# Kernel optimization log

Hardware: AMD Instinct MI355X
Metric: run time of the kernel (lower is better)

## Reference

```python
import jax, jax.numpy as jnp
import numpy as np

NUM_CLASSES = 256
FEATURE_DIM = 768
BATCH = 128
SIM_BALANCE = 0.7
TIER1 = 50.0
TIER2 = 10.0
TOPK = 5


def _l2norm(x):
    return x / jnp.linalg.norm(x, axis=1, keepdims=True)


def build_edge_weights(class_features, context_features, w1, b1, w2, b2,
                       co_occurrence, instance_counts):
    """Vectorized, faithful translation of VisualFeatureGraph.build_graph."""
    N = class_features.shape[0]
    dt = class_features.dtype
    co = co_occurrence.astype(dt)            # [N,N], diag is 0
    cnt = instance_counts.astype(dt)         # [N]

    vs = _l2norm(class_features) @ _l2norm(class_features).T    # visual_sim [N,N]
    cs = _l2norm(context_features) @ _l2norm(context_features).T  # context_sim
    combined = SIM_BALANCE * vs + (1.0 - SIM_BALANCE) * cs

    # ---- Tier 1: co > TIER1 ----
    # sim_proj(f_i - f_j): exploit linearity of first layer: (f_i-f_j)@W1 = a_i - a_j
    a = class_features @ w1                                    # [N, D/2]
    h = jax.nn.relu(a[:, None, :] - a[None, :, :] + b1)        # [N,N,D/2]
    sim_weight = jax.nn.sigmoid(h @ w2 + b2)[..., 0]           # [N,N]
    ratio = (jnp.minimum(cnt[:, None], cnt[None, :]) /
             jnp.maximum(jnp.maximum(cnt[:, None], cnt[None, :]), 1.0))
    e1 = combined * sim_weight * ratio

    # ---- Tier 2: TIER2 < co <= TIER1 ----
    # shared neighbors k: co[i,k]>T1 and co[j,k]>T1 (k=i,j auto-excluded: diag=0
    # and co[i,j]<=T1 for tier-2 pairs)
    A = (co > TIER1).astype(dt)                                # [N,N]
    M = vs * A
    shared_sum = M @ M.T                                       # sum_k vs[i,k]*vs[j,k]
    shared_cnt = A @ A.T
    avg_sim = shared_sum / jnp.maximum(shared_cnt, 1.0)
    conf = co / TIER1
    e2 = jnp.where(shared_cnt > 0,
                   conf * combined + (1.0 - conf) * avg_sim,
                   conf * combined)

    # ---- Tier 3: co <= TIER2 ----
    # top-5 neighbors per row by co-occurrence among co > TIER2 (diag=0 and
    # co[i,j]<=TIER2 for tier-3 pairs, so i and j are auto-excluded)
    top_vals, top_idx = jax.lax.top_k(co, TOPK)                # [N,K]
    valid = top_vals > TIER2                                   # [N,K]
    ii = top_idx[:, None, :, None]                             # [N,1,K,1]
    jj = top_idx[None, :, None, :]                             # [1,N,1,K]
    co_cross = co[ii, jj]                                      # co[i_neigh, j_neigh] [N,N,K,K]
    vs_cross = vs[ii, jj]
    vs_in = jnp.take_along_axis(vs, top_idx, axis=1)           # vs[i, i_neigh] [N,K]
    mask = valid[:, None, :, None] & valid[None, :, None, :] & (co_cross > 0)
    w = (top_vals[:, None, :, None] * top_vals[None, :, None, :]) / TIER1
    w = jnp.where(mask, w, 0.0)
    sim = vs_in[:, None, :, None] * vs_in[None, :, None, :] * vs_cross
    trans = jnp.sum(w * sim, axis=(2, 3))                      # [N,N]
    tot = jnp.sum(w, axis=(2, 3))
    e3 = jnp.where(tot > 0, trans / jnp.where(tot > 0, tot, 1.0), 0.1 * cs)

    tier1_mask = co > TIER1
    tier2_mask = (co > TIER2) & ~tier1_mask
    E = jnp.where(tier1_mask, e1, jnp.where(tier2_mask, e2, e3))
    E = E * (1.0 - jnp.eye(N, dtype=dt))                       # i==j skipped
    mx = jnp.max(E)
    E = jnp.where(mx > 0, E / jnp.where(mx > 0, mx, 1.0), E)
    return E


def setup_inputs() -> dict:
    key = jax.random.key(0)
    ks = jax.random.split(key, 8)
    N, D, B = NUM_CLASSES, FEATURE_DIM, BATCH
    x = jax.random.normal(ks[0], (B, N, D), dtype=jnp.float32)
    class_features = jax.random.normal(ks[1], (N, D), dtype=jnp.float32) * 0.05
    context_features = jax.random.normal(ks[2], (N, D), dtype=jnp.float32) * 0.05
    w1 = jax.random.normal(ks[3], (D, D // 2), dtype=jnp.float32) * (1.0 / np.sqrt(D))
    b1 = jnp.zeros((D // 2,), dtype=jnp.float32)
    w2 = jax.random.normal(ks[4], (D // 2, 1), dtype=jnp.float32) * (1.0 / np.sqrt(D // 2))
    b2 = jnp.zeros((1,), dtype=jnp.float32)
    co = jax.random.randint(ks[5], (N, N), 0, 121, dtype=jnp.int32)
    co = (co + co.T) // 2                                      # symmetric like update_features
    co = co * (1 - jnp.eye(N, dtype=jnp.int32))                # zero diagonal
    instance_counts = jax.random.randint(ks[6], (N,), 1, 1001, dtype=jnp.int32)
    return {"x": x, "class_features": class_features,
            "context_features": context_features,
            "w1": w1, "b1": b1, "w2": w2, "b2": b2,
            "co_occurrence": co, "instance_counts": instance_counts}


def reference(x, class_features, context_features, w1, b1, w2, b2,
              co_occurrence, instance_counts):
    E = build_edge_weights(class_features, context_features, w1, b1, w2, b2,
                           co_occurrence, instance_counts)
    # torch.bmm(E.expand(B,-1,-1), x) == einsum over shared node dim
    return x + jnp.einsum('ij,bjd->bid', E, x)
```

## Files before the change

kernel.cpp:

```cpp
#include <hip/hip_runtime.h>
#include <hip/hip_bf16.h>
#include <math.h>

#define N 256
#define D 768
#define BATCH 128

typedef float f32x4 __attribute__((ext_vector_type(4)));
typedef short bf16x8 __attribute__((ext_vector_type(8)));

static __device__ __forceinline__ unsigned short f2bf(float f) {
    unsigned int u = __float_as_uint(f);
    u += 0x7fffu + ((u >> 16) & 1u);
    return (unsigned short)(u >> 16);
}
static __device__ __forceinline__ unsigned int pack2bf(float lo, float hi) {
    unsigned int a = __float_as_uint(lo);
    unsigned int b = __float_as_uint(hi);
    a += 0x7fffu + ((a >> 16) & 1u);
    b += 0x7fffu + ((b >> 16) & 1u);
    return (a >> 16) | (b & 0xffff0000u);
}

__global__ void k_stage1(const float* __restrict__ cf, const float* __restrict__ ctx,
                         float* __restrict__ vsn, float* __restrict__ csn,
                         const float* __restrict__ w1, float* __restrict__ a,
                         const int* __restrict__ co, float* __restrict__ topv,
                         int* __restrict__ topi) {
    __shared__ float sm[2 * 64 * 33];
    int bx = blockIdx.x;
    int t = threadIdx.x;
    if (bx < 512) {
        int row = bx;
        const float* src;
        float* dst;
        if (row < N) { src = cf  + row * D;       dst = vsn + row * D; }
        else         { src = ctx + (row - N) * D; dst = csn + (row - N) * D; }
        float s = 0.f;
        for (int d = t; d < D; d += 256) { float v = src[d]; s += v * v; }
        float* red = sm;
        red[t] = s; __syncthreads();
        for (int off = 128; off > 0; off >>= 1) {
            if (t < off) red[t] += red[t + off];
            __syncthreads();
        }
        float inv = 1.0f / sqrtf(red[0]);
        for (int d = t; d < D; d += 256) dst[d] = src[d] * inv;
    } else if (bx < 608) {
        int bi = bx - 512;
        int i0 = (bi / 12) * 32, j0 = (bi % 12) * 32;
        float (*Ci)[33] = (float(*)[33])sm;
        float (*Wj)[33] = (float(*)[33])(sm + 64 * 33);
        int tx = t & 15, ty = t >> 4;
        float a00 = 0.f, a01 = 0.f, a10 = 0.f, a11 = 0.f;
        for (int k0 = 0; k0 < 768; k0 += 64) {
            #pragma unroll
            for (int s = 0; s < 8; s++) {
                int idx = s * 256 + t;
                int row = idx >> 6, kc = idx & 63;
                Ci[kc][row] = cf[(i0 + row) * 768 + k0 + kc];
                int kr = idx >> 5, col = idx & 31;
                Wj[kr][col] = w1[(k0 + kr) * 384 + j0 + col];
            }
            __syncthreads();
            #pragma unroll 4
            for (int kk = 0; kk < 64; kk++) {
                float iv0 = Ci[kk][ty * 2], iv1 = Ci[kk][ty * 2 + 1];
                float jv0 = Wj[kk][tx * 2], jv1 = Wj[kk][tx * 2 + 1];
                a00 += iv0 * jv0; a01 += iv0 * jv1;
                a10 += iv1 * jv0; a11 += iv1 * jv1;
            }
            __syncthreads();
        }
        a[(i0 + ty * 2)     * 384 + j0 + tx * 2]     = a00;
        a[(i0 + ty * 2)     * 384 + j0 + tx * 2 + 1] = a01;
        a[(i0 + ty * 2 + 1) * 384 + j0 + tx * 2]     = a10;
        a[(i0 + ty * 2 + 1) * 384 + j0 + tx * 2 + 1] = a11;
    } else {
        int lane = t & 63;
        int row = (bx - 608) * 4 + (t >> 6);
        int4 v4 = *(const int4*)(co + row * 256 + lane * 4);
        int key[4];
        key[0] = v4.x * 256 + (255 - (lane * 4 + 0));
        key[1] = v4.y * 256 + (255 - (lane * 4 + 1));
        key[2] = v4.z * 256 + (255 - (lane * 4 + 2));
        key[3] = v4.w * 256 + (255 - (lane * 4 + 3));
        for (int r = 0; r < 5; r++) {
            int best = key[0];
            #pragma unroll
            for (int e = 1; e < 4; e++) best = max(best, key[e]);
            #pragma unroll
            for (int off = 32; off > 0; off >>= 1) best = max(best, __shfl_xor(best, off, 64));
            int kidx = 255 - (best & 255);
            int val = best >> 8;
            if (lane == 0) { topv[row * 5 + r] = (float)val; topi[row * 5 + r] = kidx; }
            if ((kidx >> 2) == lane) key[kidx & 3] = -1;
        }
    }
}

__global__ void k_gram2(const float* __restrict__ vsn, const float* __restrict__ csn,
                        float* __restrict__ vs, float* __restrict__ cs) {
    int bx = blockIdx.x;
    const float* S = (bx >= 64) ? csn : vsn;
    float* O       = (bx >= 64) ? cs  : vs;
    int bi = bx & 63;
    int i0 = (bi >> 3) * 32, j0 = (bi & 7) * 32;
    __shared__ float Li[64][33], Lj[64][33];
    int t = threadIdx.x;
    int tx = t & 15, ty = t >> 4;
    float a00 = 0.f, a01 = 0.f, a10 = 0.f, a11 = 0.f;
    for (int k0 = 0; k0 < 768; k0 += 64) {
        #pragma unroll
        for (int s = 0; s < 8; s++) {
            int idx = s * 256 + t;
            int row = idx >> 6, kc = idx & 63;
            Li[kc][row] = S[(i0 + row) * 768 + k0 + kc];
            Lj[kc][row] = S[(j0 + row) * 768 + k0 + kc];
        }
        __syncthreads();
        #pragma unroll 4
        for (int kk = 0; kk < 64; kk++) {
            float iv0 = Li[kk][ty * 2], iv1 = Li[kk][ty * 2 + 1];
            float jv0 = Lj[kk][tx * 2], jv1 = Lj[kk][tx * 2 + 1];
            a00 += iv0 * jv0; a01 += iv0 * jv1;
            a10 += iv1 * jv0; a11 += iv1 * jv1;
        }
        __syncthreads();
    }
    O[(i0 + ty * 2)     * 256 + j0 + tx * 2]     = a00;
    O[(i0 + ty * 2)     * 256 + j0 + tx * 2 + 1] = a01;
    O[(i0 + ty * 2 + 1) * 256 + j0 + tx * 2]     = a10;
    O[(i0 + ty * 2 + 1) * 256 + j0 + tx * 2 + 1] = a11;
}

__global__ void k_stage3(const float* __restrict__ a, const float* __restrict__ b1,
                         const float* __restrict__ w2, const float* __restrict__ b2,
                         const float* __restrict__ vs, const float* __restrict__ cs,
                         const int* __restrict__ ic, float* __restrict__ e1,
                         const int* __restrict__ co, float* __restrict__ ss,
                         float* __restrict__ sc) {
    __shared__ float sm[12800];
    int bx = blockIdx.x;
    int t = threadIdx.x;
    if (bx < 256) {
        int i0 = (bx >> 4) * 16, j0 = (bx & 15) * 16;
        float (*ai)[388]  = (float(*)[388])sm;
        float (*ajm)[388] = (float(*)[388])(sm + 16 * 388);
        float* sw2 = sm + 2 * 16 * 388;
        for (int idx = t; idx < 16 * 96; idx += 256) {
            int r = idx / 96, c = (idx % 96) * 4;
            *(float4*)&ai[r][c] = *(const float4*)(a + (i0 + r) * 384 + c);
            float4 u  = *(const float4*)(a + (j0 + r) * 384 + c);
            float4 bb = *(const float4*)(b1 + c);
            u.x -= bb.x; u.y -= bb.y; u.z -= bb.z; u.w -= bb.w;
            *(float4*)&ajm[r][c] = u;
        }
        for (int k = t; k < 384; k += 256) sw2[k] = w2[k];
        __syncthreads();
        int tx = t & 15, ty = t >> 4;
        float s = 0.f;
        #pragma unroll 4
        for (int k4 = 0; k4 < 96; k4++) {
            float4 xv = *(const float4*)&ai[ty][k4 * 4];
            float4 yv = *(const float4*)&ajm[tx][k4 * 4];
            float4 wv = *(const float4*)&sw2[k4 * 4];
            s += fmaxf(xv.x - yv.x, 0.f) * wv.x;
            s += fmaxf(xv.y - yv.y, 0.f) * wv.y;
            s += fmaxf(xv.z - yv.z, 0.f) * wv.z;
            s += fmaxf(xv.w - yv.w, 0.f) * wv.w;
        }
        int i = i0 + ty, j = j0 + tx;
        float sig = 1.0f / (1.0f + expf(-(s + b2[0])));
        float comb = 0.7f * vs[i * 256 + j] + 0.3f * cs[i * 256 + j];
        float ci = (float)ic[i], cj = (float)ic[j];
        float mn = fminf(ci, cj), mx = fmaxf(ci, cj);
        float ratio = mn / fmaxf(mx, 1.0f);
        e1[i * 256 + j] = comb * sig * ratio;
    } else {
        int bi = bx - 256;
        int i0 = (bi >> 3) * 32, j0 = (bi & 7) * 32;
        float (*Mi)[33] = (float(*)[33])sm;
        float (*Ai)[33] = (float(*)[33])(sm + 2112);
        float (*Mj)[33] = (float(*)[33])(sm + 4224);
        float (*Aj)[33] = (float(*)[33])(sm + 6336);
        int tx = t & 15, ty = t >> 4;
        float s00=0.f,s01=0.f,s10=0.f,s11=0.f;
        float c00=0.f,c01=0.f,c10=0.f,c11=0.f;
        for (int k0 = 0; k0 < 256; k0 += 64) {
            #pragma unroll
            for (int s = 0; s < 8; s++) {
                int idx = s * 256 + t;
                int row = idx >> 6, kc = idx & 63;
                int civ = co[(i0 + row) * 256 + k0 + kc];
                float aa = civ > 50 ? 1.f : 0.f;
                Ai[kc][row] = aa;
                Mi[kc][row] = aa * vs[(i0 + row) * 256 + k0 + kc];
                int cjv = co[(j0 + row) * 256 + k0 + kc];
                float ab = cjv > 50 ? 1.f : 0.f;
                Aj[kc][row] = ab;
                Mj[kc][row] = ab * vs[(j0 + row) * 256 + k0 + kc];
            }
            __syncthreads();
            #pragma unroll 4
            for (int kk = 0; kk < 64; kk++) {
                float mi0 = Mi[kk][ty*2], mi1 = Mi[kk][ty*2+1];
                float ai0 = Ai[kk][ty*2], ai1 = Ai[kk][ty*2+1];
                float mj0 = Mj[kk][tx*2], mj1 = Mj[kk][tx*2+1];
                float aj0 = Aj[kk][tx*2], aj1 = Aj[kk][tx*2+1];
                s00 += mi0*mj0; s01 += mi0*mj1; s10 += mi1*mj0; s11 += mi1*mj1;
                c00 += ai0*aj0; c01 += ai0*aj1; c10 += ai1*aj0; c11 += ai1*aj1;
            }
            __syncthreads();
        }
        ss[(i0+ty*2)  *256 + j0+tx*2]   = s00; ss[(i0+ty*2)  *256 + j0+tx*2+1] = s01;
        ss[(i0+ty*2+1)*256 + j0+tx*2]   = s10; ss[(i0+ty*2+1)*256 + j0+tx*2+1] = s11;
        sc[(i0+ty*2)  *256 + j0+tx*2]   = c00; sc[(i0+ty*2)  *256 + j0+tx*2+1] = c01;
        sc[(i0+ty*2+1)*256 + j0+tx*2]   = c10; sc[(i0+ty*2+1)*256 + j0+tx*2+1] = c11;
    }
}

__global__ void k_assemble(const int* __restrict__ co, const float* __restrict__ vs,
                           const float* __restrict__ cs, const float* __restrict__ e1,
                           const float* __restrict__ ss, const float* __restrict__ sc,
                           const float* __restrict__ topv, const int* __restrict__ topi,
                           float* __restrict__ E, float* __restrict__ partials) {
    int i = blockIdx.x, j = threadIdx.x;
    int cij = co[i * 256 + j];
    float e;
    if (i == j) {
        e = 0.f;
    } else if (cij > 50) {
        e = e1[i * 256 + j];
    } else if (cij > 10) {
        float conf = (float)cij / 50.0f;
        float comb = 0.7f * vs[i * 256 + j] + 0.3f * cs[i * 256 + j];
        float cnt = sc[i * 256 + j];
        float avg = ss[i * 256 + j] / fmaxf(cnt, 1.f);
        e = (cnt > 0.f) ? conf * comb + (1.f - conf) * avg : conf * comb;
    } else {
        float tvi[5], tvj[5]; int tii[5], tij[5];
        #pragma unroll
        for (int k = 0; k < 5; k++) {
            tvi[k] = topv[i * 5 + k]; tii[k] = topi[i * 5 + k];
            tvj[k] = topv[j * 5 + k]; tij[k] = topi[j * 5 + k];
        }
        float trans = 0.f, tot = 0.f;
        #pragma unroll
        for (int k = 0; k < 5; k++) {
            if (!(tvi[k] > 10.f)) continue;
            float vin_i = vs[i * 256 + tii[k]];
            #pragma unroll
            for (int l = 0; l < 5; l++) {
                if (!(tvj[l] > 10.f)) continue;
                int cc = co[tii[k] * 256 + tij[l]];
                if (cc <= 0) continue;
                float w = tvi[k] * tvj[l] / 50.f;
                float sim = vin_i * vs[j * 256 + tij[l]] * vs[tii[k] * 256 + tij[l]];
                trans += w * sim; tot += w;
            }
        }
        e = (tot > 0.f) ? trans / tot : 0.1f * cs[i * 256 + j];
    }
    E[i * 256 + j] = e;
    __shared__ float red[256];
    red[j] = e; __syncthreads();
    for (int off = 128; off > 0; off >>= 1) {
        if (j < off) red[j] = fmaxf(red[j], red[j + off]);
        __syncthreads();
    }
    if (j == 0) partials[i] = red[0];
}

__global__ void k_ep(const float* __restrict__ E, const float* __restrict__ partials,
                     unsigned short* __restrict__ Ep) {
    __shared__ float red[256];
    int t = threadIdx.x;
    red[t] = partials[t]; __syncthreads();
    for (int off = 128; off > 0; off >>= 1) {
        if (t < off) red[t] = fmaxf(red[t], red[t + off]);
        __syncthreads();
    }
    float mx = red[0];
    float s = (mx > 0.f) ? 1.0f / mx : 1.0f;
    int base = (blockIdx.x * 256 + t) * 4;
    float4 e4 = *(const float4*)(E + base);
    float ev[4] = {e4.x, e4.y, e4.z, e4.w};
    unsigned short o[4];
    #pragma unroll
    for (int q = 0; q < 4; q++) {
        int g = base + q;
        float v = s * ev[q] + (((g >> 8) == (g & 255)) ? 1.0f : 0.0f);
        o[q] = f2bf(v);
    }
    uint2 w;
    w.x = (unsigned int)o[0] | ((unsigned int)o[1] << 16);
    w.y = (unsigned int)o[2] | ((unsigned int)o[3] << 16);
    *(uint2*)(Ep + base) = w;
}

#define EINS_BUFB 4736

#define EIN_BODY(KT, BB, XR, bvC, bvN)                                          \
  {                                                                             \
    uint4 pv;                                                                   \
    pv.x = pack2bf(XR[0].x, XR[0].y);                                           \
    pv.y = pack2bf(XR[0].z, XR[0].w);                                           \
    pv.z = pack2bf(XR[1].x, XR[1].y);                                           \
    pv.w = pack2bf(XR[1].z, XR[1].w);                                           \
    *(uint4*)((char*)xs + (BB) + wbyte) = pv;                                   \
    __syncthreads();                                                            \
    if ((KT) < 7) {                                                             \
      _Pragma("unroll")                                                         \
      for (int nf = 0; nf < 4; nf++)                                            \
        bvN[nf] = *(const uint4*)(eprow + (nf << 12) + ((KT) + 1) * 32);        \
    }                                                                           \
    if ((KT) < 6) {                                                             \
      const float* xn = xb + (size_t)((KT) + 2) * 32 * 768;                     \
      XR[0] = *(const float4*)xn;                                               \
      XR[1] = *(const float4*)(xn + 4);                                         \
    }                                                                           \
    uint2 a0[4], a1[4];                                                         \
    _Pragma("unroll")                                                           \
    for (int g = 0; g < 4; g++) {                                               \
      unsigned ag = ra + (BB) + g * 1184;                                       \
      asm volatile("ds_read_b64_tr_b16 %0, %1" : "=v"(a0[g]) : "v"(ag));        \
      asm volatile("ds_read_b64_tr_b16 %0, %1 offset:144" : "=v"(a1[g]) : "v"(ag)); \
    }                                                                           \
    asm volatile("s_waitcnt lgkmcnt(0)" ::: "memory");                          \
    __builtin_amdgcn_sched_barrier(0);                                          \
    _Pragma("unroll")                                                           \
    for (int mf = 0; mf < 4; mf++) {                                            \
      union { uint2 u[2]; bf16x8 v; } af;                                       \
      af.u[0] = a0[mf]; af.u[1] = a1[mf];                                       \
      _Pragma("unroll")                                                         \
      for (int nf = 0; nf < 4; nf++)                                            \
        acc[mf][nf] = __builtin_amdgcn_mfma_f32_16x16x32_bf16(                  \
            af.v, *(const bf16x8*)&bvC[nf], acc[mf][nf], 0, 0, 0);              \
    }                                                                           \
  }

__global__ __launch_bounds__(256, 3) void k_einsum_tr(
    const unsigned short* __restrict__ Ep, const float* __restrict__ x,
    float* __restrict__ out) {
    extern __shared__ unsigned short xs[];
    int t = threadIdx.x;
    int b = blockIdx.y;
    int d0 = blockIdx.x * 64;
    int lane = t & 63, w = t >> 6;
    int l15 = lane & 15, lq = lane >> 4;

    int dh = t & 7, kr = t >> 3;
    const float* xb = x + ((size_t)b * 256) * 768 + (size_t)kr * 768 + d0 + dh * 8;
    unsigned wbyte = (unsigned)((dh >> 1) * 1184 + (kr >> 2) * 144 + (kr & 3) * 32 + (dh & 1) * 16);
    unsigned ra = (unsigned)(lq * 288 + l15 * 8);

    const unsigned short* eprow = Ep + (((w * 64 + l15) << 8) + lq * 8);

    f32x4 acc[4][4];
    #pragma unroll
    for (int mf = 0; mf < 4; mf++)
        #pragma unroll
        for (int nf = 0; nf < 4; nf++)
            #pragma unroll
            for (int e = 0; e < 4; e++) acc[mf][nf][e] = 0.f;

    float4 xA[2], xB[2];
    xA[0] = *(const float4*)xb;
    xA[1] = *(const float4*)(xb + 4);
    xB[0] = *(const float4*)(xb + 32 * 768);
    xB[1] = *(const float4*)(xb + 32 * 768 + 4);
    uint4 bv0[4], bv1[4];
    #pragma unroll
    for (int nf = 0; nf < 4; nf++) bv0[nf] = *(const uint4*)(eprow + (nf << 12));

    #pragma unroll
    for (int k2 = 0; k2 < 4; k2++) {
        EIN_BODY(2 * k2,     0,         xA, bv0, bv1)
        EIN_BODY(2 * k2 + 1, EINS_BUFB, xB, bv1, bv0)
    }

    float* ob = out + ((size_t)b * 256) * 768 + d0;
    #pragma unroll
    for (int mf = 0; mf < 4; mf++) {
        #pragma unroll
        for (int nf = 0; nf < 4; nf++) {
            int i = w * 64 + nf * 16 + l15;
            int d = mf * 16 + lq * 4;
            *(float4*)(ob + (size_t)i * 768 + d) = *(float4*)&acc[mf][nf];
        }
    }
}

extern "C" void kernel_launch(void* const* d_in, const int* in_sizes, int n_in,
                              void* d_out, int out_size, void* d_ws, size_t ws_size,
                              hipStream_t stream) {
    const float* x   = (const float*)d_in[0];
    const float* cf  = (const float*)d_in[1];
    const float* ctx = (const float*)d_in[2];
    const float* w1  = (const float*)d_in[3];
    const float* b1  = (const float*)d_in[4];
    const float* w2  = (const float*)d_in[5];
    const float* b2  = (const float*)d_in[6];
    const int*   co  = (const int*)d_in[7];
    const int*   ic  = (const int*)d_in[8];
    float* out = (float*)d_out;

    float* ws   = (float*)d_ws;
    float* vsn  = ws;
    float* csn  = vsn + 196608;
    float* a    = csn + 196608;
    float* vs   = a + 98304;
    float* cs   = vs + 65536;
    float* e1   = cs + 65536;
    float* ss   = e1 + 65536;
    float* sc   = ss + 65536;
    float* E    = sc + 65536;
    float* topv = E + 65536;
    int*   topi = (int*)(topv + 1280);
    float* partials = (float*)(topi + 1280);
    unsigned short* Ep = (unsigned short*)(partials + 256);

    k_stage1<<<672, 256, 0, stream>>>(cf, ctx, vsn, csn, w1, a, co, topv, topi);
    k_gram2<<<128, 256, 0, stream>>>(vsn, csn, vs, cs);
    k_stage3<<<320, 256, 0, stream>>>(a, b1, w2, b2, vs, cs, ic, e1, co, ss, sc);
    k_assemble<<<256, 256, 0, stream>>>(co, vs, cs, e1, ss, sc, topv, topi, E, partials);
    k_ep<<<64, 256, 0, stream>>>(E, partials, Ep);
    k_einsum_tr<<<dim3(12, BATCH), 256, 2 * EINS_BUFB, stream>>>(Ep, x, out);
}
```

Measured before the change: 288.2 us.

## Stage full x tile transposed in LDS and drop double-buffered transpose reads

New measurement: 289.0 us. About the same (+0.3%).

```diff
diff --git a/kernel.cpp b/kernel.cpp
--- a/kernel.cpp
+++ b/kernel.cpp
@@ -299,85 +299,63 @@
     *(uint2*)(Ep + base) = w;
 }
 
-#define EINS_BUFB 4736
-
-#define EIN_BODY(KT, BB, XR, bvC, bvN)                                          \
-  {                                                                             \
-    uint4 pv;                                                                   \
-    pv.x = pack2bf(XR[0].x, XR[0].y);                                           \
-    pv.y = pack2bf(XR[0].z, XR[0].w);                                           \
-    pv.z = pack2bf(XR[1].x, XR[1].y);                                           \
-    pv.w = pack2bf(XR[1].z, XR[1].w);                                           \
-    *(uint4*)((char*)xs + (BB) + wbyte) = pv;                                   \
-    __syncthreads();                                                            \
-    if ((KT) < 7) {                                                             \
-      _Pragma("unroll")                                                         \
-      for (int nf = 0; nf < 4; nf++)                                            \
-        bvN[nf] = *(const uint4*)(eprow + (nf << 12) + ((KT) + 1) * 32);        \
-    }                                                                           \
-    if ((KT) < 6) {                                                             \
-      const float* xn = xb + (size_t)((KT) + 2) * 32 * 768;                     \
-      XR[0] = *(const float4*)xn;                                               \
-      XR[1] = *(const float4*)(xn + 4);                                         \
-    }                                                                           \
-    uint2 a0[4], a1[4];                                                         \
-    _Pragma("unroll")                                                           \
-    for (int g = 0; g < 4; g++) {                                               \
-      unsigned ag = ra + (BB) + g * 1184;                                       \
-      asm volatile("ds_read_b64_tr_b16 %0, %1" : "=v"(a0[g]) : "v"(ag));        \
-      asm volatile("ds_read_b64_tr_b16 %0, %1 offset:144" : "=v"(a1[g]) : "v"(ag)); \
-    }                                                                           \
-    asm volatile("s_waitcnt lgkmcnt(0)" ::: "memory");                          \
-    __builtin_amdgcn_sched_barrier(0);                                          \
-    _Pragma("unroll")                                                           \
-    for (int mf = 0; mf < 4; mf++) {                                            \
-      union { uint2 u[2]; bf16x8 v; } af;                                       \
-      af.u[0] = a0[mf]; af.u[1] = a1[mf];                                       \
-      _Pragma("unroll")                                                         \
-      for (int nf = 0; nf < 4; nf++)                                            \
-        acc[mf][nf] = __builtin_amdgcn_mfma_f32_16x16x32_bf16(                  \
-            af.v, *(const bf16x8*)&bvC[nf], acc[mf][nf], 0, 0, 0);              \
-    }                                                                           \
-  }
-
-__global__ __launch_bounds__(256, 3) void k_einsum_tr(
+__global__ __launch_bounds__(256) void k_einsum_bf(
     const unsigned short* __restrict__ Ep, const float* __restrict__ x,
     float* __restrict__ out) {
-    extern __shared__ unsigned short xs[];
+    __shared__ __align__(16) unsigned short xt[64 * 264];
     int t = threadIdx.x;
     int b = blockIdx.y;
     int d0 = blockIdx.x * 64;
     int lane = t & 63, w = t >> 6;
     int l15 = lane & 15, lq = lane >> 4;
 
-    int dh = t & 7, kr = t >> 3;
-    const float* xb = x + ((size_t)b * 256) * 768 + (size_t)kr * 768 + d0 + dh * 8;
-    unsigned wbyte = (unsigned)((dh >> 1) * 1184 + (kr >> 2) * 144 + (kr & 3) * 32 + (dh & 1) * 16);
-    unsigned ra = (unsigned)(lq * 288 + l15 * 8);
+    int dl = t & 63;
+    int ko = t >> 6;
+    const float* xb = x + ((size_t)b * 256 + ko * 8) * 768 + d0 + dl;
+
+    float v[8][8];
+    #pragma unroll
+    for (int kt = 0; kt < 8; kt++)
+        #pragma unroll
+        for (int s = 0; s < 8; s++)
+            v[kt][s] = xb[((size_t)kt * 32 + s) * 768];
+    #pragma unroll
+    for (int kt = 0; kt < 8; kt++) {
+        uint4 pv;
+        pv.x = pack2bf(v[kt][0], v[kt][1]);
+        pv.y = pack2bf(v[kt][2], v[kt][3]);
+        pv.z = pack2bf(v[kt][4], v[kt][5]);
+        pv.w = pack2bf(v[kt][6], v[kt][7]);
+        *(uint4*)&xt[dl * 264 + kt * 32 + ko * 8] = pv;
+    }
+    __syncthreads();
+
+    f32x4 acc[4][4];
+    #pragma unroll
+    for (int mf = 0; mf < 4; mf++)
+        #pragma unroll
+        for (int nf = 0; nf < 4; nf++)
+            #pragma unroll
+            for (int e = 0; e < 4; e++) acc[mf][nf][e] = 0.f;
 
     const unsigned short* eprow = Ep + (((w * 64 + l15) << 8) + lq * 8);
 
-    f32x4 acc[4][4];
-    #pragma unroll
-    for (int mf = 0; mf < 4; mf++)
+    #pragma unroll
+    for (int kt = 0; kt < 8; kt++) {
+        uint4 bv[4];
         #pragma unroll
         for (int nf = 0; nf < 4; nf++)
-            #pragma unroll
-            for (int e = 0; e < 4; e++) acc[mf][nf][e] = 0.f;
-
-    float4 xA[2], xB[2];
-    xA[0] = *(const float4*)xb;
-    xA[1] = *(const float4*)(xb + 4);
-    xB[0] = *(const float4*)(xb + 32 * 768);
-    xB[1] = *(const float4*)(xb + 32 * 768 + 4);
-    uint4 bv0[4], bv1[4];
-    #pragma unroll
-    for (int nf = 0; nf < 4; nf++) bv0[nf] = *(const uint4*)(eprow + (nf << 12));
-
-    #pragma unroll
-    for (int k2 = 0; k2 < 4; k2++) {
-        EIN_BODY(2 * k2,     0,         xA, bv0, bv1)
-        EIN_BODY(2 * k2 + 1, EINS_BUFB, xB, bv1, bv0)
+            bv[nf] = *(const uint4*)(eprow + (nf << 12) + kt * 32);
+        bf16x8 af[4];
+        #pragma unroll
+        for (int g = 0; g < 4; g++)
+            af[g] = *(const bf16x8*)&xt[(g * 16 + l15) * 264 + kt * 32 + lq * 8];
+        #pragma unroll
+        for (int mf = 0; mf < 4; mf++)
+            #pragma unroll
+            for (int nf = 0; nf < 4; nf++)
+                acc[mf][nf] = __builtin_amdgcn_mfma_f32_16x16x32_bf16(
+                    af[mf], *(const bf16x8*)&bv[nf], acc[mf][nf], 0, 0, 0);
     }
 
     float* ob = out + ((size_t)b * 256) * 768 + d0;
@@ -426,5 +404,5 @@
     k_stage3<<<320, 256, 0, stream>>>(a, b1, w2, b2, vs, cs, ic, e1, co, ss, sc);
     k_assemble<<<256, 256, 0, stream>>>(co, vs, cs, e1, ss, sc, topv, topi, E, partials);
     k_ep<<<64, 256, 0, stream>>>(E, partials, Ep);
-    k_einsum_tr<<<dim3(12, BATCH), 256, 2 * EINS_BUFB, stream>>>(Ep, x, out);
-}
+    k_einsum_bf<<<dim3(12, BATCH), 256, 0, stream>>>(Ep, x, out);
+}
```
